# Performance work log

Hardware: AMD Instinct MI355X
Metric: run time of the kernel (lower is better)

Reference implementation:

```python
import jax, jax.numpy as jnp
import numpy as np
from jax import lax

EPS = 1e-5
DN = ('NCHW', 'OIHW', 'NCHW')


def _bn(x, gamma, beta, mean, var):
    # eval-mode BatchNorm2d over channel dim (axis=1)
    s = gamma / jnp.sqrt(var + EPS)
    return x * s[None, :, None, None] + (beta - mean * s)[None, :, None, None]


def setup_inputs() -> dict:
    key = jax.random.key(0)
    ks = jax.random.split(key, 12)
    B, Cin, C, H, W, NC = 128, 2048, 512, 14, 14, 200
    return {
        'feature': jax.random.normal(ks[0], (B, Cin, H, W), jnp.float32),
        'w_reduce': jax.random.normal(ks[1], (C, Cin, 1, 1), jnp.float32) * 0.02,
        'b_reduce': jax.random.normal(ks[2], (C,), jnp.float32) * 0.02,
        'bn1_gamma': jnp.ones((C,), jnp.float32),
        'bn1_beta': jnp.zeros((C,), jnp.float32),
        'bn1_mean': jax.random.normal(ks[3], (C,), jnp.float32) * 0.02,
        'bn1_var': jax.random.uniform(ks[4], (C,), jnp.float32),
        'w3': jax.random.normal(ks[5], (C, C, 3, 3), jnp.float32) * 0.02,
        'b3': jax.random.normal(ks[6], (C,), jnp.float32) * 0.02,
        'bn2_gamma': jnp.ones((C,), jnp.float32),
        'bn2_beta': jnp.zeros((C,), jnp.float32),
        'bn2_mean': jax.random.normal(ks[7], (C,), jnp.float32) * 0.02,
        'bn2_var': jax.random.uniform(ks[8], (C,), jnp.float32),
        'fc1_w': jax.random.normal(ks[9], (NC, C), jnp.float32) * 0.02,
        'fc1_b': jnp.zeros((NC,), jnp.float32),
        'fc2_w': jax.random.normal(ks[10], (NC, NC), jnp.float32) * 0.02,
        'fc2_b': jnp.zeros((NC,), jnp.float32),
    }


def reference(feature, w_reduce, b_reduce, bn1_gamma, bn1_beta, bn1_mean, bn1_var,
              w3, b3, bn2_gamma, bn2_beta, bn2_mean, bn2_var,
              fc1_w, fc1_b, fc2_w, fc2_b):
    B, _, H, W = feature.shape
    C = w_reduce.shape[0]  # 512
    # reduce: 1x1 conv + BN + ReLU
    f = lax.conv_general_dilated(feature, w_reduce, (1, 1), 'VALID', dimension_numbers=DN)
    f = f + b_reduce[None, :, None, None]
    f = jax.nn.relu(_bn(f, bn1_gamma, bn1_beta, bn1_mean, bn1_var))
    x = f.reshape(B, C, H * W)  # [B, 512, 196]
    # channel affinity + softmax(-xxt) over last dim (= the per-row loop)
    xxt = jnp.einsum('bcn,bdn->bcd', x, x)  # [B, 512, 512]
    a = jax.nn.softmax(-xxt, axis=2)
    y = jnp.einsum('bcd,bdn->bcn', a, x).reshape(B, C, H, W)
    # conv3: 3x3 conv + BN + ReLU + global avg pool
    z = lax.conv_general_dilated(y, w3, (1, 1), 'SAME', dimension_numbers=DN)
    z = z + b3[None, :, None, None]
    z = jax.nn.relu(_bn(z, bn2_gamma, bn2_beta, bn2_mean, bn2_var))
    z = jnp.mean(z, axis=(2, 3))  # [B, 512]
    # fc_channel: Linear -> ReLU -> Linear
    h = jax.nn.relu(z @ fc1_w.T + fc1_b)
    sf = h @ fc2_w.T + fc2_b
    return sf
```

## Files before the change

### kernel.cpp

```cpp
#include <hip/hip_runtime.h>

typedef __attribute__((ext_vector_type(8))) short bf16x8;
typedef __attribute__((ext_vector_type(4))) float f32x4;
typedef __attribute__((ext_vector_type(4))) short short4v;
typedef __attribute__((ext_vector_type(2))) short short2v;

__device__ __forceinline__ unsigned short f2bf(float x){
  unsigned u = __float_as_uint(x);
  return (unsigned short)((u + 0x7FFFu + ((u>>16)&1u)) >> 16);
}
__device__ __forceinline__ float bf2f(unsigned short b){
  return __uint_as_float(((unsigned)b)<<16);
}

typedef const __attribute__((address_space(1))) void* gas_t;
typedef __attribute__((address_space(3))) void* las_t;
__device__ __forceinline__ void gl16(const void* g, void* l){
  __builtin_amdgcn_global_load_lds((gas_t)g, (las_t)l, 16, 0, 0);
}

static constexpr size_t O_FHI  = 0;
static constexpr size_t O_FLO  = 102760448;
static constexpr size_t O_XHI  = 205520896;
static constexpr size_t O_XLO  = 239075328;
static constexpr size_t O_XT   = 272629760;
static constexpr size_t O_AMAT = 301989888;
static constexpr size_t O_WH   = 369098752;
static constexpr size_t O_WL   = 371195904;
static constexpr size_t O_W3B  = 373293056;
static constexpr size_t O_PAR  = 378011648;
static constexpr size_t O_FC1T = 378019840;
static constexpr size_t O_FC2T = 378429440;
static constexpr size_t O_ZBAR = 378589440;

__global__ __launch_bounds__(256) void k_prep(
    const float* wr, unsigned short* wh, unsigned short* wl,
    const float* w3, unsigned short* w3c,
    const float* fc1w, float* fc1T, const float* fc2w, float* fc2T,
    const float* br, const float* g1, const float* be1, const float* m1, const float* v1,
    const float* b3, const float* g2, const float* be2, const float* m2, const float* v2,
    float* par, unsigned short* xhi, unsigned short* xlo){
  int blk = blockIdx.x, t = threadIdx.x;
  if (blk < 4096){
    int idx = blk*256 + t;
    int c = idx >> 11, k = idx & 2047;
    float v = wr[(size_t)c*2048 + k];
    unsigned short h = f2bf(v);
    wh[(size_t)c*2048+k] = h; wl[(size_t)c*2048+k] = f2bf(v - bf2f(h));
  } else if (blk < 13312){
    int i = (blk-4096)*256 + t;
    int co = i / 4608, k = i - co*4608;
    int ci0b = k / 576, r2 = k - ci0b*576;
    int tap = r2 >> 6, cio = r2 & 63;
    w3c[(((size_t)ci0b*9+tap)*512+co)*64+cio] =
        f2bf(w3[((size_t)co*512 + ci0b*64+cio)*9 + tap]);
  } else if (blk < 13712){
    int i = (blk-13312)*256 + t;
    int k = i/200, j = i - k*200;
    fc1T[i] = fc1w[j*512+k];
  } else if (blk < 13869){
    int i = (blk-13712)*256 + t;
    if (i < 40000){ int k = i/200, j = i - k*200; fc2T[i] = fc2w[j*200+k]; }
  } else if (blk < 13871){
    int c = (blk-13869)*256 + t;
    if (c < 512){
      float s1 = g1[c]*rsqrtf(v1[c]+1e-5f);
      par[c] = s1; par[512+c] = (br[c]-m1[c])*s1 + be1[c];
      float s2 = g2[c]*rsqrtf(v2[c]+1e-5f);
      par[1024+c] = s2; par[1536+c] = (b3[c]-m2[c])*s2 + be2[c];
    }
  } else {
    int rr = (blk-13871)*256 + t;
    float4 z = {0.f,0.f,0.f,0.f};
    float4* a = (float4*)(xhi + (size_t)rr*256 + 192);
    float4* bq = (float4*)(xlo + (size_t)rr*256 + 192);
    #pragma unroll
    for (int q=0;q<8;++q){ a[q]=z; bq[q]=z; }
  }
}

__global__ __launch_bounds__(256) void k_featT(const float* __restrict__ feat,
        unsigned short* __restrict__ fhi, unsigned short* __restrict__ flo){
  __shared__ float tile[64][33];
  int b = blockIdx.z;
  int ci0 = blockIdx.y*64, p0 = blockIdx.x*32;
  int t = threadIdx.x;
  int j = t & 31, i0 = t >> 5;
  for (int rep=0; rep<8; ++rep){
    int i = rep*8 + i0;
    int p = p0 + j;
    tile[i][j] = (p<196) ? feat[((size_t)b*2048 + ci0 + i)*196 + p] : 0.f;
  }
  __syncthreads();
  int j2 = t & 31;
  int jj0 = t >> 5;
  for (int rep=0; rep<4; ++rep){
    int jj = rep*8 + jj0;
    int p = p0 + jj;
    if (p < 196){
      float v0 = tile[2*j2][jj], v1 = tile[2*j2+1][jj];
      unsigned short h0 = f2bf(v0), h1 = f2bf(v1);
      unsigned short l0 = f2bf(v0 - bf2f(h0)), l1 = f2bf(v1 - bf2f(h1));
      size_t o = ((size_t)b*196 + p)*2048 + ci0 + 2*j2;
      short2v hv; hv[0]=(short)h0; hv[1]=(short)h1;
      short2v lv; lv[0]=(short)l0; lv[1]=(short)l1;
      *(short2v*)(fhi + o) = hv;
      *(short2v*)(flo + o) = lv;
    }
  }
}

__global__ __launch_bounds__(256, 2) void k_conv1(
    const unsigned short* __restrict__ fhi, const unsigned short* __restrict__ flo,
    const unsigned short* __restrict__ wh,  const unsigned short* __restrict__ wl,
    const float* __restrict__ par,
    unsigned short* __restrict__ xhi, unsigned short* __restrict__ xlo,
    unsigned short* __restrict__ xT){
  __shared__ char lds[65536];
  char* BUF0 = lds;
  char* BUF1 = lds + 32768;
  int lin = blockIdx.x;
  int sz  = (lin&7)*98 + (lin>>3);
  int mt = sz&3;
  int gt = sz>>2;
  int c0 = mt*128;
  size_t g0 = (size_t)gt*128;
  int t = threadIdx.x, lane = t&63, wid = t>>6, wm = wid&1, wn = wid>>1;
  int fq = lane>>4, fr = lane&15;
  f32x4 acc[4][4] = {};

  auto STAGE1 = [&](int it, char* buf){
    #pragma unroll
    for (int jj=0; jj<6; ++jj){
      int arr = jj>>1;
      int g = t + ((jj&1)<<8);
      int row = g>>2;
      int cs = ((g&3) ^ ((row>>1)&3))*8;
      const unsigned short* src;
      if (arr==0)      src = wh  + (size_t)(c0+row)*2048 + it*32 + cs;
      else if (arr==1) src = wl  + (size_t)(c0+row)*2048 + it*32 + cs;
      else             src = fhi + (g0+row)*2048 + it*32 + cs;
      gl16(src, buf + arr*8192 + g*16);
    }
  };
  auto STAGE2 = [&](int it, char* buf){
    #pragma unroll
    for (int jj=0; jj<2; ++jj){
      int g = t + (jj<<8);
      int row = g>>2;
      int cs = ((g&3) ^ ((row>>1)&3))*8;
      gl16(flo + (g0+row)*2048 + it*32 + cs, buf + 24576 + g*16);
    }
  };

  STAGE1(0, BUF0);
  STAGE2(0, BUF0);

  for (int it=0; it<64; ++it){
    char* cur = (it&1) ? BUF1 : BUF0;
    char* nxt = (it&1) ? BUF0 : BUF1;
    asm volatile("s_waitcnt vmcnt(2)" ::: "memory");
    __builtin_amdgcn_s_barrier();
    __builtin_amdgcn_sched_barrier(0);
    bf16x8 ah[4], al[4], bh[4];
    #pragma unroll
    for (int m=0;m<4;++m){
      int row = wm*64 + m*16 + fr;
      int off = row*64 + ((fq*16) ^ (((row>>1)&3)<<4));
      ah[m] = *(const bf16x8*)(cur + off);
      al[m] = *(const bf16x8*)(cur + 8192 + off);
    }
    #pragma unroll
    for (int n=0;n<4;++n){
      int row = wn*64 + n*16 + fr;
      int off = row*64 + ((fq*16) ^ (((row>>1)&3)<<4));
      bh[n] = *(const bf16x8*)(cur + 16384 + off);
    }
    if (it < 63) STAGE1(it+1, nxt);
    asm volatile("s_waitcnt lgkmcnt(0)" ::: "memory");
    __builtin_amdgcn_sched_barrier(0);
    __builtin_amdgcn_s_setprio(1);
    #pragma unroll
    for (int n=0;n<4;++n)
      #pragma unroll
      for (int m=0;m<4;++m){
        acc[m][n] = __builtin_amdgcn_mfma_f32_16x16x32_bf16(ah[m], bh[n], acc[m][n],0,0,0);
        acc[m][n] = __builtin_amdgcn_mfma_f32_16x16x32_bf16(al[m], bh[n], acc[m][n],0,0,0);
      }
    __builtin_amdgcn_s_setprio(0);
    if (it < 63) { asm volatile("s_waitcnt vmcnt(6)" ::: "memory"); }
    else         { asm volatile("s_waitcnt vmcnt(0)" ::: "memory"); }
    __builtin_amdgcn_s_barrier();
    __builtin_amdgcn_sched_barrier(0);
    bf16x8 bl[4];
    #pragma unroll
    for (int n=0;n<4;++n){
      int row = wn*64 + n*16 + fr;
      int off = row*64 + ((fq*16) ^ (((row>>1)&3)<<4));
      bl[n] = *(const bf16x8*)(cur + 24576 + off);
    }
    if (it < 63) STAGE2(it+1, nxt);
    asm volatile("s_waitcnt lgkmcnt(0)" ::: "memory");
    __builtin_amdgcn_sched_barrier(0);
    __builtin_amdgcn_s_setprio(1);
    #pragma unroll
    for (int n=0;n<4;++n)
      #pragma unroll
      for (int m=0;m<4;++m)
        acc[m][n] = __builtin_amdgcn_mfma_f32_16x16x32_bf16(ah[m], bl[n], acc[m][n],0,0,0);
    __builtin_amdgcn_s_setprio(0);
  }

  const float* s1 = par; const float* t1 = par+512;
  for (int m=0;m<4;++m){
    int cb = c0 + wm*64 + m*16 + fq*4;
    float sc[4], sh[4];
    for (int j=0;j<4;++j){ sc[j]=s1[cb+j]; sh[j]=t1[cb+j]; }
    for (int n=0;n<4;++n){
      int gg = (int)g0 + wn*64 + n*16 + fr;
      int b = gg/196, p = gg - b*196;
      unsigned short hs[4];
      for (int j=0;j<4;++j){
        float v = fmaxf(acc[m][n][j]*sc[j]+sh[j], 0.f);
        unsigned short h = f2bf(v);
        hs[j] = h;
        size_t ic = (size_t)b*512 + cb + j;
        xhi[ic*256 + p] = h;
        xlo[ic*256 + p] = f2bf(v - bf2f(h));
      }
      *(short4v*)(xT + ((size_t)b*224 + p)*512 + cb) = *(short4v*)hs;
    }
  }
}

__global__ __launch_bounds__(256) void k_xxt(const unsigned short* __restrict__ xhi,
        const unsigned short* __restrict__ xlo, float* __restrict__ xxt){
  __shared__ char lds[32768];
  char* Als = lds; char* Bls = lds + 16384;
  int lin = blockIdx.x;
  int sz  = (lin&7)*160 + (lin>>3);
  int b = sz/10, sub = sz - b*10;
  unsigned mtp = (3u<<18)|(2u<<16)|(2u<<14)|(1u<<12)|(1u<<10)|(1u<<8)|(0u<<6)|(0u<<4)|(0u<<2)|0u;
  unsigned ntp = (3u<<18)|(3u<<16)|(2u<<14)|(3u<<12)|(2u<<10)|(1u<<8)|(3u<<6)|(2u<<4)|(1u<<2)|0u;
  int mt = (mtp>>(2*sub))&3, nt = (ntp>>(2*sub))&3;
  int c0 = mt*128, d0 = nt*128;
  int t = threadIdx.x, lane = t&63, wid = t>>6, wm = wid&1, wn = wid>>1;
  int fq = lane>>4, fr = lane&15;
  f32x4 acc[4][4] = {};
  for (int it=0; it<12; ++it){
    int seg = it>>2, kk0 = (it&3)*64;
    const unsigned short* As = (seg<2) ? xhi : xlo;
    const unsigned short* Bs = (seg==1) ? xlo : xhi;
    __syncthreads();
    #pragma unroll
    for (int r=0;r<4;++r){
      int L = r*256 + t;
      int row = L>>3, cs = ((L&7)^(row&7))*8;
      gl16(As + ((size_t)b*512 + c0 + row)*256 + kk0 + cs, Als + L*16);
      gl16(Bs + ((size_t)b*512 + d0 + row)*256 + kk0 + cs, Bls + L*16);
    }
    __syncthreads();
    #pragma unroll
    for (int ks=0; ks<2; ++ks){
      int kb = ks*64 + fq*16;
      bf16x8 af[4];
      #pragma unroll
      for (int m=0;m<4;++m){
        int row = wm*64 + m*16 + fr;
        af[m] = *(const bf16x8*)(Als + row*128 + (kb ^ ((row&7)<<4)));
      }
      #pragma unroll
      for (int n=0;n<4;++n){
        int row = wn*64 + n*16 + fr;
        bf16x8 bff = *(const bf16x8*)(Bls + row*128 + (kb ^ ((row&7)<<4)));
        #pragma unroll
        for (int m=0;m<4;++m)
          acc[m][n] = __builtin_amdgcn_mfma_f32_16x16x32_bf16(af[m], bff, acc[m][n],0,0,0);
      }
    }
  }
  for (int m=0;m<4;++m){
    int cb = c0 + wm*64 + m*16 + fq*4;
    for (int n=0;n<4;++n){
      int d = d0 + wn*64 + n*16 + fr;
      *(float4*)(xxt + ((size_t)b*512 + d)*512 + cb) = *(float4*)&acc[m][n];
    }
  }
  if (mt != nt){
    for (int m=0;m<4;++m){
      int cb = c0 + wm*64 + m*16 + fq*4;
      for (int n=0;n<4;++n){
        int d = d0 + wn*64 + n*16 + fr;
        for (int jj=0;jj<4;++jj)
          xxt[((size_t)b*512 + cb + jj)*512 + d] = acc[m][n][jj];
      }
    }
  }
}

__global__ __launch_bounds__(256) void k_softmax(const float* __restrict__ xxt, unsigned short* __restrict__ amat){
  int row = blockIdx.x*4 + (threadIdx.x>>6);
  int lane = threadIdx.x & 63;
  const float* src = xxt + (size_t)row*512 + lane*8;
  float4 v0 = *(const float4*)src;
  float4 v1 = *(const float4*)(src+4);
  float mn = fminf(fminf(fminf(v0.x,v0.y),fminf(v0.z,v0.w)),
                   fminf(fminf(v1.x,v1.y),fminf(v1.z,v1.w)));
  for (int m=32; m; m>>=1) mn = fminf(mn, __shfl_xor(mn, m, 64));
  float e[8];
  e[0]=__expf(mn-v0.x); e[1]=__expf(mn-v0.y); e[2]=__expf(mn-v0.z); e[3]=__expf(mn-v0.w);
  e[4]=__expf(mn-v1.x); e[5]=__expf(mn-v1.y); e[6]=__expf(mn-v1.z); e[7]=__expf(mn-v1.w);
  float s = e[0]+e[1]+e[2]+e[3]+e[4]+e[5]+e[6]+e[7];
  for (int m=32; m; m>>=1) s += __shfl_xor(s, m, 64);
  float inv = 1.f/s;
  short4v p0, p1;
  for (int q=0;q<4;++q) p0[q] = (short)f2bf(e[q]*inv);
  for (int q=0;q<4;++q) p1[q] = (short)f2bf(e[4+q]*inv);
  unsigned short* dst = amat + (size_t)row*512 + lane*8;
  *(short4v*)dst = p0;
  *(short4v*)(dst+4) = p1;
}

__global__ __launch_bounds__(256) void k_pv(const unsigned short* __restrict__ amat,
        const unsigned short* __restrict__ xT, unsigned short* __restrict__ ypad){
  __shared__ char lds[30720];
  char* Als = lds; char* Bls = lds + 16384;
  int lin = blockIdx.x, per = gridDim.x>>3;
  int sz  = (lin&7)*per + (lin>>3);
  int b = sz>>3, sub = sz&7, mt = sub>>1, nt = sub&1;
  int c0 = mt*128, n0 = nt*112;
  int t = threadIdx.x, lane = t&63, wid = t>>6;
  int fq = lane>>4, fr = lane&15;
  {
    int r = t;
    int hi = r>>4, lo2 = r&15;
    if (hi==0||hi==15||lo2==0||lo2==15){
      float4 z = {0.f,0.f,0.f,0.f};
      float4* pz = (float4*)(ypad + (((size_t)b*8 + sub)*256 + r)*64);
      #pragma unroll
      for (int q=0;q<8;++q) pz[q] = z;
    }
  }
  f32x4 acc[2][7] = {};
  for (int it=0; it<8; ++it){
    int k0 = it*64;
    __syncthreads();
    #pragma unroll
    for (int r=0;r<4;++r){
      int L = r*256 + t;
      int row = L>>3, cs = ((L&7)^(row&7))*8;
      gl16(amat + ((size_t)b*512 + c0 + row)*512 + k0 + cs, Als + L*16);
    }
    #pragma unroll
    for (int r=0;r<4;++r){
      int L = r*256 + t;
      if (L < 896){
        int row = L>>3, cs = ((L&7)^(row&7))*8;
        gl16(xT + ((size_t)b*224 + n0 + row)*512 + k0 + cs, Bls + L*16);
      }
    }
    __syncthreads();
    #pragma unroll
    for (int ks=0; ks<2; ++ks){
      int kb = ks*64 + fq*16;
      bf16x8 af[2];
      #pragma unroll
      for (int m=0;m<2;++m){
        int row = wid*32 + m*16 + fr;
        af[m] = *(const bf16x8*)(Als + row*128 + (kb ^ ((row&7)<<4)));
      }
      #pragma unroll
      for (int n=0;n<7;++n){
        int row = n*16 + fr;
        bf16x8 bff = *(const bf16x8*)(Bls + row*128 + (kb ^ ((row&7)<<4)));
        #pragma unroll
        for (int m=0;m<2;++m)
          acc[m][n] = __builtin_amdgcn_mfma_f32_16x16x32_bf16(af[m], bff, acc[m][n],0,0,0);
      }
    }
  }
  for (int m=0;m<2;++m){
    int cb = c0 + wid*32 + m*16 + fq*4;
    int ci0b = cb>>6, cio = cb&63;
    for (int n=0;n<7;++n){
      int p = n0 + n*16 + fr;
      if (p < 196){
        int hh = p/14, wwp = p - hh*14;
        int prow = (hh+1)*16 + (wwp+1);
        short4v pk;
        for (int j=0;j<4;++j) pk[j] = (short)f2bf(acc[m][n][j]);
        *(short4v*)(ypad + (((size_t)b*8 + ci0b)*256 + prow)*64 + cio) = pk;
      }
    }
  }
}

__global__ __launch_bounds__(512, 2) void k_conv3(const unsigned short* __restrict__ ypad,
        const unsigned short* __restrict__ w3c, const float* __restrict__ par,
        float* __restrict__ zbar){
  __shared__ char lds[65536];
  char* WIN = lds;
  char* AB0 = lds + 32768;
  char* AB1 = lds + 49152;
  int bx = blockIdx.x;
  int xcd = bx&7, jj2 = bx>>3;
  int b = xcd*16 + (jj2>>2), cot = jj2&3;
  int c0 = cot*128;
  int t = threadIdx.x, lane = t&63, w = t>>6;
  int wm = w>>2, wn = (w>>1)&1, wks = w&1;
  int fq = lane>>4, fr = lane&15;
  int frB = (fr<14) ? fr : 13;
  bool pok = (fr<14);
  f32x4 acc[4][7] = {};
  for (int ci0=0; ci0<8; ++ci0){
    const unsigned short* wsrc = ypad + ((size_t)(b*8 + ci0)*256)*64;
    #pragma unroll
    for (int r=0;r<4;++r){
      int L = r*512 + t;
      int row = L>>3, cs = ((L&7)^(row&7))*8;
      gl16(wsrc + row*64 + cs, WIN + L*16);
    }
    {
      const unsigned short* asrc = w3c + ((size_t)(ci0*9 + 0)*512 + c0)*64;
      #pragma unroll
      for (int r=0;r<2;++r){
        int L = r*512 + t;
        int row = L>>3, cs = ((L&7)^(row&7))*8;
        gl16(asrc + row*64 + cs, AB0 + L*16);
      }
    }
    __syncthreads();
    for (int tap=0; tap<9; ++tap){
      char* Acur = (tap&1) ? AB1 : AB0;
      char* Anxt = (tap&1) ? AB0 : AB1;
      if (tap < 8){
        const unsigned short* asrc = w3c + ((size_t)(ci0*9 + tap+1)*512 + c0)*64;
        #pragma unroll
        for (int r=0;r<2;++r){
          int L = r*512 + t;
          int row = L>>3, cs = ((L&7)^(row&7))*8;
          gl16(asrc + row*64 + cs, Anxt + L*16);
        }
      }
      int kh = tap/3, kw = tap - kh*3;
      bf16x8 ah[4];
      #pragma unroll
      for (int m=0;m<4;++m){
        int row = wm*64 + m*16 + fr;
        ah[m] = *(const bf16x8*)(Acur + row*128 + (((wks*4+fq)^(row&7))<<4));
      }
      int col = frB + kw;
      __builtin_amdgcn_s_setprio(1);
      #pragma unroll
      for (int n=0;n<7;++n){
        int prow = (wn*7 + n + kh)*16 + col;
        bf16x8 bf = *(const bf16x8*)(WIN + prow*128 + (((wks*4+fq)^(prow&7))<<4));
        #pragma unroll
        for (int m=0;m<4;++m)
          acc[m][n] = __builtin_amdgcn_mfma_f32_16x16x32_bf16(ah[m], bf, acc[m][n],0,0,0);
      }
      __builtin_amdgcn_s_setprio(0);
      __syncthreads();
    }
  }
  #pragma unroll
  for (int half=0; half<2; ++half){
    if (wks){
      #pragma unroll
      for (int m2=0;m2<2;++m2)
        #pragma unroll
        for (int n=0;n<7;++n)
          *(f32x4*)(lds + (((size_t)((wm*2+wn)*14 + m2*7 + n))*64 + lane)*16) = acc[half*2+m2][n];
    }
    __syncthreads();
    if (!wks){
      #pragma unroll
      for (int m2=0;m2<2;++m2)
        #pragma unroll
        for (int n=0;n<7;++n){
          f32x4 o = *(const f32x4*)(lds + (((size_t)((wm*2+wn)*14 + m2*7 + n))*64 + lane)*16);
          acc[half*2+m2][n] += o;
        }
    }
    __syncthreads();
  }
  const float* s2 = par+1024; const float* t2 = par+1536;
  float ps[4][4];
  if (!wks){
    #pragma unroll
    for (int m=0;m<4;++m){
      int cb = c0 + wm*64 + m*16 + fq*4;
      #pragma unroll
      for (int j=0;j<4;++j){
        float sc = s2[cb+j], sh = t2[cb+j];
        float s = 0.f;
        #pragma unroll
        for (int n=0;n<7;++n)
          s += fmaxf(acc[m][n][j]*sc + sh, 0.f);
        ps[m][j] = pok ? s : 0.f;
      }
    }
    #pragma unroll
    for (int off=1; off<16; off<<=1)
      #pragma unroll
      for (int m=0;m<4;++m)
        #pragma unroll
        for (int j=0;j<4;++j)
          ps[m][j] += __shfl_xor(ps[m][j], off, 64);
  }
  float* part = (float*)lds;
  if (!wks && fr == 0){
    #pragma unroll
    for (int m=0;m<4;++m)
      #pragma unroll
      for (int j=0;j<4;++j)
        part[wn*128 + wm*64 + m*16 + fq*4 + j] = ps[m][j];
  }
  __syncthreads();
  if (t < 128)
    zbar[(size_t)b*512 + c0 + t] = part[t] + part[128 + t];
}

__global__ __launch_bounds__(256) void k_fc(const float* __restrict__ zbar,
        const float* __restrict__ fc1T, const float* __restrict__ fc1b,
        const float* __restrict__ fc2T, const float* __restrict__ fc2b,
        float* __restrict__ out){
  __shared__ float zb[512];
  __shared__ float hl[200];
  int b = blockIdx.x, t = threadIdx.x;
  zb[t]     = zbar[(size_t)b*512 + t]       * (1.f/196.f);
  zb[t+256] = zbar[(size_t)b*512 + t + 256] * (1.f/196.f);
  __syncthreads();
  if (t < 200){
    float acc = fc1b[t];
    for (int k=0;k<512;++k) acc += zb[k]*fc1T[k*200+t];
    hl[t] = fmaxf(acc, 0.f);
  }
  __syncthreads();
  if (t < 200){
    float acc = fc2b[t];
    for (int k=0;k<200;++k) acc += hl[k]*fc2T[k*200+t];
    out[(size_t)b*200 + t] = acc;
  }
}

extern "C" void kernel_launch(void* const* d_in, const int* in_sizes, int n_in,
                              void* d_out, int out_size, void* d_ws, size_t ws_size,
                              hipStream_t stream) {
  const float* feature  = (const float*)d_in[0];
  const float* w_reduce = (const float*)d_in[1];
  const float* b_reduce = (const float*)d_in[2];
  const float* g1  = (const float*)d_in[3];
  const float* be1 = (const float*)d_in[4];
  const float* m1  = (const float*)d_in[5];
  const float* v1  = (const float*)d_in[6];
  const float* w3  = (const float*)d_in[7];
  const float* b3  = (const float*)d_in[8];
  const float* g2  = (const float*)d_in[9];
  const float* be2 = (const float*)d_in[10];
  const float* m2  = (const float*)d_in[11];
  const float* v2  = (const float*)d_in[12];
  const float* fc1w = (const float*)d_in[13];
  const float* fc1b = (const float*)d_in[14];
  const float* fc2w = (const float*)d_in[15];
  const float* fc2b = (const float*)d_in[16];

  char* ws = (char*)d_ws;
  unsigned short* fhi  = (unsigned short*)(ws + O_FHI);
  unsigned short* flo  = (unsigned short*)(ws + O_FLO);
  float*          xxt  = (float*)(ws + O_FHI);
  unsigned short* xhi  = (unsigned short*)(ws + O_XHI);
  unsigned short* xlo  = (unsigned short*)(ws + O_XLO);
  unsigned short* ypad = (unsigned short*)(ws + O_XLO);
  unsigned short* xT   = (unsigned short*)(ws + O_XT);
  unsigned short* amat = (unsigned short*)(ws + O_AMAT);
  unsigned short* wh   = (unsigned short*)(ws + O_WH);
  unsigned short* wl   = (unsigned short*)(ws + O_WL);
  unsigned short* w3c  = (unsigned short*)(ws + O_W3B);
  float* par  = (float*)(ws + O_PAR);
  float* fc1T = (float*)(ws + O_FC1T);
  float* fc2T = (float*)(ws + O_FC2T);
  float* zbar = (float*)(ws + O_ZBAR);

  k_prep<<<14127, 256, 0, stream>>>(w_reduce, wh, wl, w3, w3c,
      fc1w, fc1T, fc2w, fc2T,
      b_reduce, g1, be1, m1, v1, b3, g2, be2, m2, v2, par, xhi, xlo);

  k_featT<<<dim3(7,32,128), 256, 0, stream>>>(feature, fhi, flo);
  k_conv1<<<784, 256, 0, stream>>>(fhi, flo, wh, wl, par, xhi, xlo, xT);

  k_xxt<<<1280, 256, 0, stream>>>(xhi, xlo, xxt);
  k_softmax<<<16384, 256, 0, stream>>>(xxt, amat);

  k_pv<<<1024, 256, 0, stream>>>(amat, xT, ypad);
  k_conv3<<<512, 512, 0, stream>>>(ypad, w3c, par, zbar);
  k_fc<<<128, 256, 0, stream>>>(zbar, fc1T, fc1b, fc2T, fc2b, (float*)d_out);
}
```

Before: 606.9 us.

## Enlarge conv1 block tile to 256x256 with three-stage split-operand pipeline

Reworks the 1x1 reduce-conv GEMM so each 512-thread block computes a 256x256 output tile with 128 KB of double-buffered LDS, instead of a 128x128 tile per 256-thread block. The weight-lo operand now gets its own load stage, so each K step runs three MFMA phases, each overlapped with the next step's loads. The larger tile doubles operand reuse per byte fetched from global memory. In exchange the grid drops to 196 blocks, fewer than the GPU's compute units, with one block per CU and heavier register pressure from 128 accumulator floats per thread.

```diff
diff --git a/kernel.cpp b/kernel.cpp
--- a/kernel.cpp
+++ b/kernel.cpp
@@ -110,110 +110,133 @@
   }
 }
 
-__global__ __launch_bounds__(256, 2) void k_conv1(
+__global__ __launch_bounds__(512, 2) void k_conv1(
     const unsigned short* __restrict__ fhi, const unsigned short* __restrict__ flo,
     const unsigned short* __restrict__ wh,  const unsigned short* __restrict__ wl,
     const float* __restrict__ par,
     unsigned short* __restrict__ xhi, unsigned short* __restrict__ xlo,
     unsigned short* __restrict__ xT){
-  __shared__ char lds[65536];
+  __shared__ char lds[131072];
   char* BUF0 = lds;
-  char* BUF1 = lds + 32768;
+  char* BUF1 = lds + 65536;
   int lin = blockIdx.x;
-  int sz  = (lin&7)*98 + (lin>>3);
-  int mt = sz&3;
-  int gt = sz>>2;
-  int c0 = mt*128;
-  size_t g0 = (size_t)gt*128;
-  int t = threadIdx.x, lane = t&63, wid = t>>6, wm = wid&1, wn = wid>>1;
+  int mt = lin & 1;
+  int gt = lin >> 1;
+  int c0 = mt*256;
+  size_t g0 = (size_t)gt*256;
+  int t = threadIdx.x, lane = t&63, wid = t>>6;
+  int wm = wid>>2, wn = wid&3;
   int fq = lane>>4, fr = lane&15;
-  f32x4 acc[4][4] = {};
-
-  auto STAGE1 = [&](int it, char* buf){
-    #pragma unroll
-    for (int jj=0; jj<6; ++jj){
-      int arr = jj>>1;
-      int g = t + ((jj&1)<<8);
+  f32x4 acc[8][4] = {};
+
+  auto STG1 = [&](int it, char* buf){
+    #pragma unroll
+    for (int j=0;j<4;++j){
+      int g = t + ((j&1)<<9);
       int row = g>>2;
       int cs = ((g&3) ^ ((row>>1)&3))*8;
-      const unsigned short* src;
-      if (arr==0)      src = wh  + (size_t)(c0+row)*2048 + it*32 + cs;
-      else if (arr==1) src = wl  + (size_t)(c0+row)*2048 + it*32 + cs;
-      else             src = fhi + (g0+row)*2048 + it*32 + cs;
-      gl16(src, buf + arr*8192 + g*16);
+      if (j<2) gl16(wh  + (size_t)(c0+row)*2048 + it*32 + cs, buf + g*16);
+      else     gl16(fhi + (g0+row)*2048 + it*32 + cs, buf + 32768 + g*16);
     }
   };
-  auto STAGE2 = [&](int it, char* buf){
-    #pragma unroll
-    for (int jj=0; jj<2; ++jj){
-      int g = t + (jj<<8);
+  auto STG2 = [&](int it, char* buf){
+    #pragma unroll
+    for (int j=0;j<2;++j){
+      int g = t + (j<<9);
       int row = g>>2;
       int cs = ((g&3) ^ ((row>>1)&3))*8;
-      gl16(flo + (g0+row)*2048 + it*32 + cs, buf + 24576 + g*16);
+      gl16(flo + (g0+row)*2048 + it*32 + cs, buf + 49152 + g*16);
     }
   };
-
-  STAGE1(0, BUF0);
-  STAGE2(0, BUF0);
+  auto STG3 = [&](int it, char* buf){
+    #pragma unroll
+    for (int j=0;j<2;++j){
+      int g = t + (j<<9);
+      int row = g>>2;
+      int cs = ((g&3) ^ ((row>>1)&3))*8;
+      gl16(wl + (size_t)(c0+row)*2048 + it*32 + cs, buf + 16384 + g*16);
+    }
+  };
+
+  STG1(0, BUF0); STG2(0, BUF0); STG3(0, BUF0);
+  asm volatile("s_waitcnt vmcnt(4)" ::: "memory");
+  __builtin_amdgcn_s_barrier();
+  __builtin_amdgcn_sched_barrier(0);
 
   for (int it=0; it<64; ++it){
     char* cur = (it&1) ? BUF1 : BUF0;
     char* nxt = (it&1) ? BUF0 : BUF1;
-    asm volatile("s_waitcnt vmcnt(2)" ::: "memory");
-    __builtin_amdgcn_s_barrier();
-    __builtin_amdgcn_sched_barrier(0);
-    bf16x8 ah[4], al[4], bh[4];
-    #pragma unroll
-    for (int m=0;m<4;++m){
-      int row = wm*64 + m*16 + fr;
-      int off = row*64 + ((fq*16) ^ (((row>>1)&3)<<4));
-      ah[m] = *(const bf16x8*)(cur + off);
-      al[m] = *(const bf16x8*)(cur + 8192 + off);
+    bool more = (it < 63);
+    bf16x8 ah[8], bh[4];
+    #pragma unroll
+    for (int m=0;m<8;++m){
+      int row = wm*128 + m*16 + fr;
+      ah[m] = *(const bf16x8*)(cur + row*64 + ((fq*16) ^ (((row>>1)&3)<<4)));
     }
     #pragma unroll
     for (int n=0;n<4;++n){
       int row = wn*64 + n*16 + fr;
-      int off = row*64 + ((fq*16) ^ (((row>>1)&3)<<4));
-      bh[n] = *(const bf16x8*)(cur + 16384 + off);
-    }
-    if (it < 63) STAGE1(it+1, nxt);
+      bh[n] = *(const bf16x8*)(cur + 32768 + row*64 + ((fq*16) ^ (((row>>1)&3)<<4)));
+    }
+    if (more) STG1(it+1, nxt);
     asm volatile("s_waitcnt lgkmcnt(0)" ::: "memory");
     __builtin_amdgcn_sched_barrier(0);
     __builtin_amdgcn_s_setprio(1);
     #pragma unroll
     for (int n=0;n<4;++n)
       #pragma unroll
-      for (int m=0;m<4;++m){
+      for (int m=0;m<8;++m)
         acc[m][n] = __builtin_amdgcn_mfma_f32_16x16x32_bf16(ah[m], bh[n], acc[m][n],0,0,0);
-        acc[m][n] = __builtin_amdgcn_mfma_f32_16x16x32_bf16(al[m], bh[n], acc[m][n],0,0,0);
-      }
     __builtin_amdgcn_s_setprio(0);
-    if (it < 63) { asm volatile("s_waitcnt vmcnt(6)" ::: "memory"); }
-    else         { asm volatile("s_waitcnt vmcnt(0)" ::: "memory"); }
+    if (more) { asm volatile("s_waitcnt vmcnt(6)" ::: "memory"); }
+    else      { asm volatile("s_waitcnt vmcnt(2)" ::: "memory"); }
     __builtin_amdgcn_s_barrier();
     __builtin_amdgcn_sched_barrier(0);
     bf16x8 bl[4];
     #pragma unroll
     for (int n=0;n<4;++n){
       int row = wn*64 + n*16 + fr;
-      int off = row*64 + ((fq*16) ^ (((row>>1)&3)<<4));
-      bl[n] = *(const bf16x8*)(cur + 24576 + off);
-    }
-    if (it < 63) STAGE2(it+1, nxt);
+      bl[n] = *(const bf16x8*)(cur + 49152 + row*64 + ((fq*16) ^ (((row>>1)&3)<<4)));
+    }
+    if (more) STG2(it+1, nxt);
     asm volatile("s_waitcnt lgkmcnt(0)" ::: "memory");
     __builtin_amdgcn_sched_barrier(0);
     __builtin_amdgcn_s_setprio(1);
     #pragma unroll
     for (int n=0;n<4;++n)
       #pragma unroll
-      for (int m=0;m<4;++m)
+      for (int m=0;m<8;++m)
         acc[m][n] = __builtin_amdgcn_mfma_f32_16x16x32_bf16(ah[m], bl[n], acc[m][n],0,0,0);
     __builtin_amdgcn_s_setprio(0);
+    if (more) { asm volatile("s_waitcnt vmcnt(6)" ::: "memory"); }
+    else      { asm volatile("s_waitcnt vmcnt(0)" ::: "memory"); }
+    __builtin_amdgcn_s_barrier();
+    __builtin_amdgcn_sched_barrier(0);
+    bf16x8 al[8];
+    #pragma unroll
+    for (int m=0;m<8;++m){
+      int row = wm*128 + m*16 + fr;
+      al[m] = *(const bf16x8*)(cur + 16384 + row*64 + ((fq*16) ^ (((row>>1)&3)<<4)));
+    }
+    if (more) STG3(it+1, nxt);
+    asm volatile("s_waitcnt lgkmcnt(0)" ::: "memory");
+    __builtin_amdgcn_sched_barrier(0);
+    __builtin_amdgcn_s_setprio(1);
+    #pragma unroll
+    for (int n=0;n<4;++n)
+      #pragma unroll
+      for (int m=0;m<8;++m)
+        acc[m][n] = __builtin_amdgcn_mfma_f32_16x16x32_bf16(al[m], bh[n], acc[m][n],0,0,0);
+    __builtin_amdgcn_s_setprio(0);
+    if (more) { asm volatile("s_waitcnt vmcnt(4)" ::: "memory"); }
+    else      { asm volatile("s_waitcnt vmcnt(0)" ::: "memory"); }
+    __builtin_amdgcn_s_barrier();
+    __builtin_amdgcn_sched_barrier(0);
   }
 
   const float* s1 = par; const float* t1 = par+512;
-  for (int m=0;m<4;++m){
-    int cb = c0 + wm*64 + m*16 + fq*4;
+  for (int m=0;m<8;++m){
+    int cb = c0 + wm*128 + m*16 + fq*4;
     float sc[4], sh[4];
     for (int j=0;j<4;++j){ sc[j]=s1[cb+j]; sh[j]=t1[cb+j]; }
     for (int n=0;n<4;++n){
@@ -587,7 +610,7 @@
       b_reduce, g1, be1, m1, v1, b3, g2, be2, m2, v2, par, xhi, xlo);
 
   k_featT<<<dim3(7,32,128), 256, 0, stream>>>(feature, fhi, flo);
-  k_conv1<<<784, 256, 0, stream>>>(fhi, flo, wh, wl, par, xhi, xlo, xT);
+  k_conv1<<<196, 512, 0, stream>>>(fhi, flo, wh, wl, par, xhi, xlo, xT);
 
   k_xxt<<<1280, 256, 0, stream>>>(xhi, xlo, xxt);
   k_softmax<<<16384, 256, 0, stream>>>(xxt, amat);
```

Measured after the change: 628.7 us. +3.6%, slower.
